# Kernel optimization log

Measured on AMD Instinct MI355X. Metric: run time of the kernel, lower is better.

Reference implementation:

```python
import jax, jax.numpy as jnp
import numpy as np


def setup_inputs() -> dict:
    key = jax.random.key(0)
    ks = jax.random.split(key, 8)
    B, H, W, C = 4, 64, 64, 256
    d = C // 8  # 32
    s = 0.02
    return {
        "x": jax.random.normal(ks[0], (B, H, W, C), dtype=jnp.float32),
        "Wq": jax.random.normal(ks[1], (C, d), dtype=jnp.float32) * s,
        "bq": jnp.zeros((d,), dtype=jnp.float32),
        "Wk": jax.random.normal(ks[2], (C, d), dtype=jnp.float32) * s,
        "bk": jnp.zeros((d,), dtype=jnp.float32),
        "Wv": jax.random.normal(ks[3], (C, C), dtype=jnp.float32) * s,
        "bv": jnp.zeros((C,), dtype=jnp.float32),
        "gamma": jnp.zeros((1,), dtype=jnp.float32),
    }


def reference(x, Wq, bq, Wk, bk, Wv, bv, gamma):
    B, H, W, C = x.shape
    N = H * W
    xf = x.reshape(B, N, C)                       # 1x1 conv == per-pixel matmul
    q = xf @ Wq + bq                              # [B, N, C//8]
    k = xf @ Wk + bk                              # [B, N, C//8]
    v = xf @ Wv + bv                              # [B, N, C]
    attn = jax.nn.softmax(jnp.einsum('bnd,bmd->bnm', q, k), axis=-1)  # [B, N, N]
    out = jnp.einsum('bnm,bmc->bnc', attn, v).reshape(B, H, W, C)
    return gamma * out + x
```

## Files before the change

kernel.cpp:

```cpp
#include <hip/hip_runtime.h>
#include <hip/hip_bf16.h>

typedef __bf16 bf16;
typedef __bf16 bf16x8 __attribute__((ext_vector_type(8)));
typedef float f32x4 __attribute__((ext_vector_type(4)));

static __device__ __forceinline__ f32x4 mfma16(bf16x8 a, bf16x8 b, f32x4 c) {
  return __builtin_amdgcn_mfma_f32_16x16x32_bf16(a, b, c, 0, 0, 0);
}

static __device__ __forceinline__ bf16x8 cvt8(const float* p) {
  f32x4 a0 = *(const f32x4*)p;
  f32x4 a1 = *(const f32x4*)(p + 4);
  bf16x8 r;
#pragma unroll
  for (int j = 0; j < 4; ++j) { r[j] = (bf16)a0[j]; r[4 + j] = (bf16)a1[j]; }
  return r;
}

__global__ void prep_wt(const float* __restrict__ Wq, const float* __restrict__ Wk,
                        const float* __restrict__ Wv, bf16* __restrict__ Wt) {
  int k = blockIdx.x;
  int c = threadIdx.x;
  float v;
  if (c < 32)       v = Wq[k * 32 + c];
  else if (c < 64)  v = Wk[k * 32 + (c - 32)];
  else              v = Wv[k * 256 + (c - 64)];
  Wt[c * 256 + k] = (bf16)v;
}

__global__ __launch_bounds__(256) void qkv_gemm(
    const float* __restrict__ x, const bf16* __restrict__ Wt,
    const float* __restrict__ bq, const float* __restrict__ bk,
    const float* __restrict__ bv,
    bf16* __restrict__ Qd, bf16* __restrict__ Kd, bf16* __restrict__ Vt) {
  __shared__ __align__(16) bf16 tile[64 * 72];
  int tid = threadIdx.x;
  int lane = tid & 63, w = tid >> 6;
  int lw = lane & 15, qq = lane >> 4;
  int r0 = blockIdx.x * 64;
  int bb = r0 >> 12, n0 = r0 & 4095;

  const float* arow = x + (size_t)(r0 + 16 * w + lw) * 256;
  bf16x8 a[8];
#pragma unroll
  for (int kc = 0; kc < 8; ++kc) a[kc] = cvt8(arow + kc * 32 + qq * 8);

  for (int c0 = 0; c0 < 320; c0 += 64) {
    f32x4 acc[4] = {};
#pragma unroll
    for (int kc = 0; kc < 8; ++kc)
#pragma unroll
      for (int t = 0; t < 4; ++t) {
        bf16x8 b = *(const bf16x8*)(Wt + (size_t)(c0 + 16 * t + lw) * 256 + kc * 32 + qq * 8);
        acc[t] = mfma16(a[kc], b, acc[t]);
      }
    if (c0 == 0) {
#pragma unroll
      for (int t = 0; t < 4; ++t) {
        int c = 16 * t + lw;
        float bias = (c < 32) ? bq[c] : bk[c - 32];
#pragma unroll
        for (int i = 0; i < 4; ++i) {
          int n = n0 + 16 * w + 4 * qq + i;
          bf16 hv = (bf16)(acc[t][i] + bias);
          if (c < 32) Qd[((size_t)(bb << 12) + n) * 32 + c] = hv;
          else        Kd[((size_t)(bb << 12) + n) * 32 + (c - 32)] = hv;
        }
      }
    } else {
#pragma unroll
      for (int t = 0; t < 4; ++t) {
        int cl = 16 * t + lw;
        float bias = bv[c0 - 64 + cl];
#pragma unroll
        for (int i = 0; i < 4; ++i)
          tile[cl * 72 + 16 * w + 4 * qq + i] = (bf16)(acc[t][i] + bias);
      }
      __syncthreads();
      int nl = tid & 63;
#pragma unroll
      for (int it = 0; it < 16; ++it) {
        int cl = 4 * it + w;
        Vt[((size_t)bb * 256 + (c0 - 64) + cl) * 4096 + n0 + nl] = tile[cl * 72 + nl];
      }
      __syncthreads();
    }
  }
}

__global__ __launch_bounds__(512, 2) void flash_attn(
    const bf16* __restrict__ Qd, const bf16* __restrict__ Kd,
    const bf16* __restrict__ Vt, const float* __restrict__ x,
    const float* __restrict__ gamma, float* __restrict__ out) {
  __shared__ __align__(16) bf16 Pl[2][64 * 72];
  __shared__ __align__(16) float lsum2[2][64];

  int tid = threadIdx.x;
  int lane = tid & 63, w = tid >> 6;
  int lw = lane & 15, qq = lane >> 4;
  int wr = w & 3, wc = w >> 2, chb = 32 * w;
  int bb = blockIdx.y;
  int r0 = blockIdx.x * 64;

  const bf16* Qb = Qd + ((size_t)bb << 12) * 32;
  const bf16* Kb = Kd + ((size_t)bb << 12) * 32;
  const bf16* Vb = Vt + (size_t)bb * 256 * 4096;

  bf16x8 qf = *(const bf16x8*)(Qb + (size_t)(r0 + 16 * wr + lw) * 32 + qq * 8);

  f32x4 o[4][2] = {};
  float l_part[4] = {};
  bf16x8 kbuf0[2], kbuf1[2], vbuf0[4], vbuf1[4];

#pragma unroll
  for (int t = 0; t < 2; ++t)
    kbuf0[t] = *(const bf16x8*)(Kb + (size_t)(32 * wc + 16 * t + lw) * 32 + qq * 8);
  {
    f32x4 s[2];
#pragma unroll
    for (int t = 0; t < 2; ++t) { f32x4 z = {}; s[t] = mfma16(qf, kbuf0[t], z); }
#pragma unroll
    for (int t = 0; t < 2; ++t)
#pragma unroll
      for (int i = 0; i < 4; ++i) {
        float p = __expf(s[t][i]);
        l_part[i] += p;
        Pl[0][(16 * wr + 4 * qq + i) * 72 + 32 * wc + 16 * t + lw] = (bf16)p;
      }
  }
#pragma unroll
  for (int t = 0; t < 2; ++t)
    kbuf1[t] = *(const bf16x8*)(Kb + (size_t)(64 + 32 * wc + 16 * t + lw) * 32 + qq * 8);
#pragma unroll
  for (int t = 0; t < 2; ++t)
#pragma unroll
    for (int kc = 0; kc < 2; ++kc)
      vbuf0[t * 2 + kc] = *(const bf16x8*)(Vb + (size_t)(chb + 16 * t + lw) * 4096 + kc * 32 + qq * 8);
  __syncthreads();

#define FA_BODY(J, PCUR, PNXT, KN, KC, VC, VN)                                     \
  {                                                                                \
    const int j = (J);                                                             \
    int n1 = ((j + 1) & 63) * 64, n2 = ((j + 2) & 63) * 64;                        \
    bf16x8 af[4][2];                                                               \
    _Pragma("unroll") for (int m = 0; m < 4; ++m)                                  \
      _Pragma("unroll") for (int kc = 0; kc < 2; ++kc)                             \
        af[m][kc] = *(const bf16x8*)&Pl[PCUR][(16 * m + lw) * 72 + kc * 32 + qq * 8]; \
    if (j < 63) {                                                                  \
      f32x4 s[2];                                                                  \
      _Pragma("unroll") for (int t = 0; t < 2; ++t) {                              \
        f32x4 z = {};                                                              \
        s[t] = mfma16(qf, KN[t], z);                                               \
      }                                                                            \
      _Pragma("unroll") for (int t = 0; t < 2; ++t)                                \
        _Pragma("unroll") for (int i = 0; i < 4; ++i) {                            \
          float p = __expf(s[t][i]);                                               \
          l_part[i] += p;                                                          \
          Pl[PNXT][(16 * wr + 4 * qq + i) * 72 + 32 * wc + 16 * t + lw] = (bf16)p; \
        }                                                                          \
      _Pragma("unroll") for (int t = 0; t < 2; ++t)                                \
        KC[t] = *(const bf16x8*)(Kb + (size_t)(n2 + 32 * wc + 16 * t + lw) * 32 + qq * 8); \
    }                                                                              \
    _Pragma("unroll") for (int t = 0; t < 2; ++t)                                  \
      _Pragma("unroll") for (int kc = 0; kc < 2; ++kc)                             \
        VN[t * 2 + kc] = *(const bf16x8*)(Vb + (size_t)(chb + 16 * t + lw) * 4096 + n1 + kc * 32 + qq * 8); \
    _Pragma("unroll") for (int kc = 0; kc < 2; ++kc)                               \
      _Pragma("unroll") for (int t = 0; t < 2; ++t)                                \
        _Pragma("unroll") for (int m = 0; m < 4; ++m)                              \
          o[m][t] = mfma16(af[m][kc], VC[t * 2 + kc], o[m][t]);                    \
    __syncthreads();                                                               \
  }

  for (int jj = 0; jj < 32; ++jj) {
    FA_BODY(2 * jj,     0, 1, kbuf1, kbuf0, vbuf0, vbuf1)
    FA_BODY(2 * jj + 1, 1, 0, kbuf0, kbuf1, vbuf1, vbuf0)
  }
#undef FA_BODY

#pragma unroll
  for (int i = 0; i < 4; ++i) {
    float v = l_part[i];
    v += __shfl_xor(v, 1);
    v += __shfl_xor(v, 2);
    v += __shfl_xor(v, 4);
    v += __shfl_xor(v, 8);
    if (lw == 0) lsum2[wc][16 * wr + 4 * qq + i] = v;
  }
  __syncthreads();

  float g = gamma[0];
#pragma unroll
  for (int m = 0; m < 4; ++m) {
    f32x4 la = *(const f32x4*)&lsum2[0][16 * m + 4 * qq];
    f32x4 lb = *(const f32x4*)&lsum2[1][16 * m + 4 * qq];
#pragma unroll
    for (int i = 0; i < 4; ++i) {
      float rinv = 1.f / (la[i] + lb[i]);
      int row = r0 + 16 * m + 4 * qq + i;
      size_t base = (((size_t)bb << 12) + row) * 256 + chb;
#pragma unroll
      for (int t = 0; t < 2; ++t)
        out[base + 16 * t + lw] = g * (o[m][t][i] * rinv) + x[base + 16 * t + lw];
    }
  }
}

extern "C" void kernel_launch(void* const* d_in, const int* in_sizes, int n_in,
                              void* d_out, int out_size, void* d_ws, size_t ws_size,
                              hipStream_t stream) {
  const float* x     = (const float*)d_in[0];
  const float* Wq    = (const float*)d_in[1];
  const float* bq    = (const float*)d_in[2];
  const float* Wk    = (const float*)d_in[3];
  const float* bk    = (const float*)d_in[4];
  const float* Wv    = (const float*)d_in[5];
  const float* bv    = (const float*)d_in[6];
  const float* gamma = (const float*)d_in[7];
  float* out = (float*)d_out;

  const size_t WT_E = 320 * 256;
  const size_t QK_E = (size_t)4096 * 32;
  const size_t VT_E = (size_t)256 * 4096;
  size_t full_bytes = (WT_E + 4 * 2 * QK_E + 4 * VT_E) * sizeof(bf16);

  bf16* Wt = (bf16*)d_ws;
  prep_wt<<<dim3(256), dim3(320), 0, stream>>>(Wq, Wk, Wv, Wt);

  if (ws_size >= full_bytes) {
    bf16* Qd = Wt + WT_E;
    bf16* Kd = Qd + 4 * QK_E;
    bf16* Vt = Kd + 4 * QK_E;
    qkv_gemm<<<dim3(256), dim3(256), 0, stream>>>(x, Wt, bq, bk, bv, Qd, Kd, Vt);
    flash_attn<<<dim3(64, 4), dim3(512), 0, stream>>>(Qd, Kd, Vt, x, gamma, out);
  } else {
    bf16* Qd = Wt + WT_E;
    bf16* Kd = Qd + QK_E;
    bf16* Vt = Kd + QK_E;
    for (int b = 0; b < 4; ++b) {
      const float* xb = x + (size_t)b * 4096 * 256;
      float* outb = out + (size_t)b * 4096 * 256;
      qkv_gemm<<<dim3(64), dim3(256), 0, stream>>>(xb, Wt, bq, bk, bv, Qd, Kd, Vt);
      flash_attn<<<dim3(64, 1), dim3(512), 0, stream>>>(Qd, Kd, Vt, xb, gamma, outb);
    }
  }
}
```

Baseline: 181.1 us.

## Split flash attention over channel halves and pre-swizzle weights for MFMA loads

The attention kernel now launches a third grid dimension of 2, with each block covering 128 output channels instead of 256. This halves each wave's V registers and accumulators, allowing launch_bounds of 4 blocks per CU and doubling the grid from 256 to 512 blocks. The cost is that each channel half recomputes QK^T and the exponentials. The weight prep also writes W in an MFMA-fragment-swizzled layout so each lane does a contiguous 16-byte load, and s_setprio is raised around the PV MFMAs.

Result: no change. 182.3 us (+0.7%).

```diff
diff --git a/kernel.cpp b/kernel.cpp
--- a/kernel.cpp
+++ b/kernel.cpp
@@ -19,18 +19,20 @@
 }
 
 __global__ void prep_wt(const float* __restrict__ Wq, const float* __restrict__ Wk,
-                        const float* __restrict__ Wv, bf16* __restrict__ Wt) {
+                        const float* __restrict__ Wv, bf16* __restrict__ Wf) {
   int k = blockIdx.x;
   int c = threadIdx.x;
   float v;
   if (c < 32)       v = Wq[k * 32 + c];
   else if (c < 64)  v = Wk[k * 32 + (c - 32)];
   else              v = Wv[k * 256 + (c - 64)];
-  Wt[c * 256 + k] = (bf16)v;
+  int t5 = c >> 6, ct = (c >> 4) & 3, lwc = c & 15;
+  int kc = k >> 5, qq = (k >> 3) & 3, ke = k & 7;
+  Wf[((((t5 * 8 + kc) * 4 + ct) * 64) + qq * 16 + lwc) * 8 + ke] = (bf16)v;
 }
 
 __global__ __launch_bounds__(256) void qkv_gemm(
-    const float* __restrict__ x, const bf16* __restrict__ Wt,
+    const float* __restrict__ x, const bf16* __restrict__ Wf,
     const float* __restrict__ bq, const float* __restrict__ bk,
     const float* __restrict__ bv,
     bf16* __restrict__ Qd, bf16* __restrict__ Kd, bf16* __restrict__ Vt) {
@@ -47,12 +49,13 @@
   for (int kc = 0; kc < 8; ++kc) a[kc] = cvt8(arow + kc * 32 + qq * 8);
 
   for (int c0 = 0; c0 < 320; c0 += 64) {
+    int t5 = c0 >> 6;
     f32x4 acc[4] = {};
 #pragma unroll
     for (int kc = 0; kc < 8; ++kc)
 #pragma unroll
       for (int t = 0; t < 4; ++t) {
-        bf16x8 b = *(const bf16x8*)(Wt + (size_t)(c0 + 16 * t + lw) * 256 + kc * 32 + qq * 8);
+        bf16x8 b = *(const bf16x8*)(Wf + ((size_t)(((t5 * 8 + kc) * 4 + t) * 64) + lane) * 8);
         acc[t] = mfma16(a[kc], b, acc[t]);
       }
     if (c0 == 0) {
@@ -89,7 +92,7 @@
   }
 }
 
-__global__ __launch_bounds__(512, 2) void flash_attn(
+__global__ __launch_bounds__(512, 4) void flash_attn(
     const bf16* __restrict__ Qd, const bf16* __restrict__ Kd,
     const bf16* __restrict__ Vt, const float* __restrict__ x,
     const float* __restrict__ gamma, float* __restrict__ out) {
@@ -99,7 +102,8 @@
   int tid = threadIdx.x;
   int lane = tid & 63, w = tid >> 6;
   int lw = lane & 15, qq = lane >> 4;
-  int wr = w & 3, wc = w >> 2, chb = 32 * w;
+  int wr = w & 3, wc = w >> 2;
+  int chb = (blockIdx.z << 7) + 16 * w;
   int bb = blockIdx.y;
   int r0 = blockIdx.x * 64;
 
@@ -109,9 +113,9 @@
 
   bf16x8 qf = *(const bf16x8*)(Qb + (size_t)(r0 + 16 * wr + lw) * 32 + qq * 8);
 
-  f32x4 o[4][2] = {};
+  f32x4 o[4] = {};
   float l_part[4] = {};
-  bf16x8 kbuf0[2], kbuf1[2], vbuf0[4], vbuf1[4];
+  bf16x8 kbuf0[2], kbuf1[2], vbuf0[2], vbuf1[2];
 
 #pragma unroll
   for (int t = 0; t < 2; ++t)
@@ -133,10 +137,8 @@
   for (int t = 0; t < 2; ++t)
     kbuf1[t] = *(const bf16x8*)(Kb + (size_t)(64 + 32 * wc + 16 * t + lw) * 32 + qq * 8);
 #pragma unroll
-  for (int t = 0; t < 2; ++t)
-#pragma unroll
-    for (int kc = 0; kc < 2; ++kc)
-      vbuf0[t * 2 + kc] = *(const bf16x8*)(Vb + (size_t)(chb + 16 * t + lw) * 4096 + kc * 32 + qq * 8);
+  for (int kc = 0; kc < 2; ++kc)
+    vbuf0[kc] = *(const bf16x8*)(Vb + (size_t)(chb + lw) * 4096 + kc * 32 + qq * 8);
   __syncthreads();
 
 #define FA_BODY(J, PCUR, PNXT, KN, KC, VC, VN)                                     \
@@ -162,13 +164,13 @@
       _Pragma("unroll") for (int t = 0; t < 2; ++t)                                \
         KC[t] = *(const bf16x8*)(Kb + (size_t)(n2 + 32 * wc + 16 * t + lw) * 32 + qq * 8); \
     }                                                                              \
-    _Pragma("unroll") for (int t = 0; t < 2; ++t)                                  \
-      _Pragma("unroll") for (int kc = 0; kc < 2; ++kc)                             \
-        VN[t * 2 + kc] = *(const bf16x8*)(Vb + (size_t)(chb + 16 * t + lw) * 4096 + n1 + kc * 32 + qq * 8); \
     _Pragma("unroll") for (int kc = 0; kc < 2; ++kc)                               \
-      _Pragma("unroll") for (int t = 0; t < 2; ++t)                                \
-        _Pragma("unroll") for (int m = 0; m < 4; ++m)                              \
-          o[m][t] = mfma16(af[m][kc], VC[t * 2 + kc], o[m][t]);                    \
+      VN[kc] = *(const bf16x8*)(Vb + (size_t)(chb + lw) * 4096 + n1 + kc * 32 + qq * 8); \
+    __builtin_amdgcn_s_setprio(1);                                                 \
+    _Pragma("unroll") for (int kc = 0; kc < 2; ++kc)                               \
+      _Pragma("unroll") for (int m = 0; m < 4; ++m)                                \
+        o[m] = mfma16(af[m][kc], VC[kc], o[m]);                                    \
+    __builtin_amdgcn_s_setprio(0);                                                 \
     __syncthreads();                                                               \
   }
 
@@ -199,9 +201,7 @@
       float rinv = 1.f / (la[i] + lb[i]);
       int row = r0 + 16 * m + 4 * qq + i;
       size_t base = (((size_t)bb << 12) + row) * 256 + chb;
-#pragma unroll
-      for (int t = 0; t < 2; ++t)
-        out[base + 16 * t + lw] = g * (o[m][t][i] * rinv) + x[base + 16 * t + lw];
+      out[base + lw] = g * (o[m][i] * rinv) + x[base + lw];
     }
   }
 }
@@ -224,24 +224,24 @@
   const size_t VT_E = (size_t)256 * 4096;
   size_t full_bytes = (WT_E + 4 * 2 * QK_E + 4 * VT_E) * sizeof(bf16);
 
-  bf16* Wt = (bf16*)d_ws;
-  prep_wt<<<dim3(256), dim3(320), 0, stream>>>(Wq, Wk, Wv, Wt);
+  bf16* Wf = (bf16*)d_ws;
+  prep_wt<<<dim3(256), dim3(320), 0, stream>>>(Wq, Wk, Wv, Wf);
 
   if (ws_size >= full_bytes) {
-    bf16* Qd = Wt + WT_E;
+    bf16* Qd = Wf + WT_E;
     bf16* Kd = Qd + 4 * QK_E;
     bf16* Vt = Kd + 4 * QK_E;
-    qkv_gemm<<<dim3(256), dim3(256), 0, stream>>>(x, Wt, bq, bk, bv, Qd, Kd, Vt);
-    flash_attn<<<dim3(64, 4), dim3(512), 0, stream>>>(Qd, Kd, Vt, x, gamma, out);
+    qkv_gemm<<<dim3(256), dim3(256), 0, stream>>>(x, Wf, bq, bk, bv, Qd, Kd, Vt);
+    flash_attn<<<dim3(64, 4, 2), dim3(512), 0, stream>>>(Qd, Kd, Vt, x, gamma, out);
   } else {
-    bf16* Qd = Wt + WT_E;
+    bf16* Qd = Wf + WT_E;
     bf16* Kd = Qd + QK_E;
     bf16* Vt = Kd + QK_E;
     for (int b = 0; b < 4; ++b) {
       const float* xb = x + (size_t)b * 4096 * 256;
       float* outb = out + (size_t)b * 4096 * 256;
-      qkv_gemm<<<dim3(64), dim3(256), 0, stream>>>(xb, Wt, bq, bk, bv, Qd, Kd, Vt);
-      flash_attn<<<dim3(64, 1), dim3(512), 0, stream>>>(Qd, Kd, Vt, xb, gamma, outb);
+      qkv_gemm<<<dim3(64), dim3(256), 0, stream>>>(xb, Wf, bq, bk, bv, Qd, Kd, Vt);
+      flash_attn<<<dim3(64, 1, 2), dim3(512), 0, stream>>>(Qd, Kd, Vt, xb, gamma, outb);
     }
   }
 }
```
